# Optimization experiments

Measured on AMD Instinct MI355X. Metric: run time of the kernel, lower is better.

## Reference

```python
import jax, jax.numpy as jnp
import numpy as np

B, L, D_MODEL, N_HEADS = 8, 256, 2048, 8
D_HEAD = D_MODEL // N_HEADS  # 256 == L, required by DeltaRuleOperator broadcasting
ALPHA0, BETA0 = 0.1, 0.9      # delta_rule_strength, 1 - strength
LN_EPS = 1e-5


def setup_inputs() -> dict:
    k = jax.random.key(0)
    ks = jax.random.split(k, 8)
    s = 0.02
    return {
        "query": jax.random.normal(ks[0], (B, L, D_MODEL), jnp.float32),
        "key": jax.random.normal(ks[1], (B, L, D_MODEL), jnp.float32),
        "value": jax.random.normal(ks[2], (B, L, D_MODEL), jnp.float32),
        "Wq": jax.random.normal(ks[3], (D_MODEL, D_MODEL), jnp.float32) * s,
        "Wk": jax.random.normal(ks[4], (D_MODEL, D_MODEL), jnp.float32) * s,
        "Wv": jax.random.normal(ks[5], (D_MODEL, D_MODEL), jnp.float32) * s,
        "Wo": jax.random.normal(ks[6], (D_MODEL, D_MODEL), jnp.float32) * s,
        "bo": jnp.zeros((D_MODEL,), jnp.float32),
        "ln_g": jnp.ones((D_MODEL,), jnp.float32),
        "ln_b": jnp.zeros((D_MODEL,), jnp.float32),
        "alpha": jnp.asarray(ALPHA0, jnp.float32),
        "beta": jnp.asarray(BETA0, jnp.float32),
    }


def reference(query, key, value, Wq, Wk, Wv, Wo, bo, ln_g, ln_b, alpha, beta):
    Bs, Ls, D = query.shape
    H, Dh = N_HEADS, D // N_HEADS

    def proj(x, W):  # torch Linear: x @ W.T, split heads -> [B,H,L,Dh]
        return (x @ W.T).reshape(Bs, Ls, H, Dh).transpose(0, 2, 1, 3)

    Q = proj(query, Wq)
    K = proj(key, Wk)
    V = proj(value, Wv)

    # DeltaRuleOperator, applied sequentially per head (buffer mutates across heads)
    kv = jnp.einsum('bhld,bhmd->bhlm', K, V)  # [B,H,L,L] with L == Dh
    kv_heads = jnp.moveaxis(kv, 1, 0)          # [H,B,L,L]

    def cs_step(cs, kv_h):
        # cumulative_state = beta*cs + alpha*detach(mean(kv)); head uses pre-update cs
        new = beta * cs + alpha * jax.lax.stop_gradient(kv_h.mean(axis=(0, 1)))
        return new, cs

    _, cs_seq = jax.lax.scan(cs_step, jnp.zeros((Dh,), query.dtype), kv_heads)  # [H,Dh]
    cs_b = cs_seq[None, :, None, :]                       # [1,H,1,Dh]
    q_mod = Q * (cs_b + alpha * (kv - cs_b))              # delta-rule modulated queries

    # elu feature map
    phi = lambda x: jax.nn.elu(x) + 1.0
    pq, pk = phi(q_mod), phi(K)

    def time_major(x):  # [B,H,L,Dh] -> [L, B*H, Dh]
        return x.reshape(Bs * H, Ls, Dh).transpose(1, 0, 2)

    pq_t, pk_t, v_t = time_major(pq), time_major(pk), time_major(V)

    def step(carry, xs):
        S, Z = carry                        # S:[N,Dh,Dh], Z:[N,Dh]
        q_i, k_i, v_i = xs                  # each [N,Dh]
        S = S + k_i[:, :, None] * v_i[:, None, :]
        Z = Z + k_i
        num = jnp.einsum('nf,nfd->nd', q_i, S)
        den = jnp.maximum(jnp.sum(q_i * Z, axis=-1), 1e-8)
        return (S, Z), num / den[:, None]

    N = Bs * H
    S0 = jnp.zeros((N, Dh, Dh), query.dtype)
    Z0 = jnp.zeros((N, Dh), query.dtype)
    _, outs = jax.lax.scan(step, (S0, Z0), (pq_t, pk_t, v_t))  # [L,N,Dh]

    attn = outs.transpose(1, 0, 2).reshape(Bs, H, Ls, Dh)
    attn = attn.transpose(0, 2, 1, 3).reshape(Bs, Ls, D)       # concat heads

    o = attn @ Wo.T + bo                  # out_proj (dropout is identity in eval)
    x = query + o                          # residual + LayerNorm
    mu = x.mean(-1, keepdims=True)
    var = jnp.mean((x - mu) ** 2, axis=-1, keepdims=True)
    return (x - mu) / jnp.sqrt(var + LN_EPS) * ln_g + ln_b
```

## Files before the change

### kernel.cpp

```cpp
#include <hip/hip_runtime.h>
#include <hip/hip_bf16.h>

using u16 = unsigned short;

typedef __bf16 bf16x8 __attribute__((ext_vector_type(8)));
typedef float  f32x4  __attribute__((ext_vector_type(4)));

__device__ __forceinline__ float b2f(u16 u) {
  union { unsigned u; float f; } v; v.u = ((unsigned)u) << 16; return v.f;
}
__device__ __forceinline__ u16 f2b(float f) {
  union { float f; unsigned u; } v; v.f = f;
  unsigned r = v.u + 0x7fffu + ((v.u >> 16) & 1u);
  return (u16)(r >> 16);
}

__device__ __forceinline__ void gld_lds16(const void* g, void* l) {
  __builtin_amdgcn_global_load_lds(
      (__attribute__((address_space(1))) void*)(unsigned long long)(g),
      (__attribute__((address_space(3))) void*)(unsigned long long)(l),
      16, 0, 0);
}

template <int EPI>
__global__ __launch_bounds__(256) void gemm_bt(
    const u16* __restrict__ A, int lda, long sA1, long sA2,
    const u16* __restrict__ B, int ldb, long sB1, long sB2,
    void* __restrict__ Cv, int ldc, long sC1, long sC2,
    int K, int HDIV,
    const float* __restrict__ den, int denLd,
    const float* __restrict__ bias, const float* __restrict__ resid) {
  __shared__ __align__(16) u16 lds[8192];
  const int t = threadIdx.x;
  const int lane = t & 63;
  const int wave = t >> 6;
  const int wm = wave >> 1, wn = wave & 1;
  const int laneM = lane & 15, quad = lane >> 4;
  const int zb = blockIdx.z / HDIV, zh = blockIdx.z % HDIV;

  int bx = blockIdx.x, by = blockIdx.y;
  if (EPI == 2) { by = (bx >= 1) ? 1 : 0; bx = (bx == 2) ? 1 : 0; }
  const int kEnd = (EPI == 3) ? ((by + 1) * 128 < K ? (by + 1) * 128 : K) : K;

  const u16* Abase = A + zb * sA1 + zh * sA2 + (long)by * 128 * lda;
  const u16* Bbase = B + zb * sB1 + zh * sB2 + (long)bx * 128 * ldb;

  const int rA = t >> 2;
  const int kc = (((t & 3) ^ ((rA >> 1) & 3)) * 8);

  f32x4 acc[4][4];
#pragma unroll
  for (int i = 0; i < 4; ++i)
#pragma unroll
    for (int j = 0; j < 4; ++j) acc[i][j] = (f32x4){0.f, 0.f, 0.f, 0.f};

  const int fragOff = laneM * 32 + ((quad ^ ((laneM >> 1) & 3)) * 8);

  for (int k0 = 0; k0 < kEnd; k0 += 32) {
    gld_lds16(Abase + (long)rA * lda + k0 + kc, &lds[t * 8]);
    gld_lds16(Abase + (long)(rA + 64) * lda + k0 + kc, &lds[2048 + t * 8]);
    gld_lds16(Bbase + (long)rA * ldb + k0 + kc, &lds[4096 + t * 8]);
    gld_lds16(Bbase + (long)(rA + 64) * ldb + k0 + kc, &lds[6144 + t * 8]);
    __syncthreads();
    bf16x8 af[4], bfv[4];
#pragma unroll
    for (int i = 0; i < 4; ++i)
      af[i] = *(const bf16x8*)&lds[(wm * 64 + i * 16) * 32 + fragOff];
#pragma unroll
    for (int j = 0; j < 4; ++j)
      bfv[j] = *(const bf16x8*)&lds[4096 + (wn * 64 + j * 16) * 32 + fragOff];
#pragma unroll
    for (int i = 0; i < 4; ++i)
#pragma unroll
      for (int j = 0; j < 4; ++j)
        acc[i][j] = __builtin_amdgcn_mfma_f32_16x16x32_bf16(af[i], bfv[j],
                                                            acc[i][j], 0, 0, 0);
    __syncthreads();
  }

  const long cOff = zb * sC1 + zh * sC2;
  const int rowB = by * 128 + wm * 64;
  const int colB = bx * 128 + wn * 64;
#pragma unroll
  for (int i = 0; i < 4; ++i) {
#pragma unroll
    for (int j = 0; j < 4; ++j) {
#pragma unroll
      for (int r = 0; r < 4; ++r) {
        const int row = rowB + i * 16 + quad * 4 + r;
        const int col = colB + j * 16 + laneM;
        const long idx = cOff + (long)row * ldc + col;
        float v = acc[i][j][r];
        if (EPI == 0) {
          ((u16*)Cv)[idx] = f2b(v);
        } else if (EPI == 1) {
          ((float*)Cv)[idx] = v;
        } else if (EPI == 2) {
          ((u16*)Cv)[idx] = f2b(col <= row ? v : 0.0f);
        } else if (EPI == 3) {
          ((u16*)Cv)[idx] = f2b(v / den[(long)blockIdx.z * denLd + row]);
        } else {
          ((float*)Cv)[idx] = v + bias[col] + resid[(long)row * ldc + col];
        }
      }
    }
  }
}

__global__ __launch_bounds__(256) void convert7(
    const float* __restrict__ s0, const float* __restrict__ s1,
    const float* __restrict__ s2, const float* __restrict__ s3,
    const float* __restrict__ s4, const float* __restrict__ s5,
    const float* __restrict__ s6, u16* __restrict__ dst) {
  long idx = (long)blockIdx.x * 256 + threadIdx.x;
  int seg = (int)(idx >> 20);
  long off = (idx & 1048575) << 2;
  const float* s;
  switch (seg) {
    case 0: s = s0; break; case 1: s = s1; break; case 2: s = s2; break;
    case 3: s = s3; break; case 4: s = s4; break; case 5: s = s5; break;
    default: s = s6;
  }
  float4 v = *(const float4*)(s + off);
  ushort4 o;
  o.x = f2b(v.x); o.y = f2b(v.y); o.z = f2b(v.z); o.w = f2b(v.w);
  *(ushort4*)(dst + (long)seg * 4194304 + off) = o;
}

__global__ __launch_bounds__(256) void kv_mean_partial(
    const float* __restrict__ kv, float* __restrict__ part) {
  int h = blockIdx.x, chunk = blockIdx.y, m = threadIdx.x;
  float acc = 0.f;
  for (int g = chunk * 128; g < chunk * 128 + 128; ++g) {
    int b = g >> 8, l = g & 255;
    acc += kv[(((long)(b * 8 + h) * 256) + l) * 256 + m];
  }
  part[(h * 16 + chunk) * 256 + m] = acc;
}

__global__ __launch_bounds__(256) void cs_kernel(
    const float* __restrict__ part, float* __restrict__ cs,
    const float* __restrict__ alphaP, const float* __restrict__ betaP) {
  int m = threadIdx.x;
  float alpha = *alphaP, beta = *betaP;
  float c = 0.f;
  for (int h = 0; h < 8; ++h) {
    cs[h * 256 + m] = c;
    float s = 0.f;
    for (int ch = 0; ch < 16; ++ch) s += part[(h * 16 + ch) * 256 + m];
    c = beta * c + alpha * (s * (1.0f / 2048.0f));
  }
}

__global__ __launch_bounds__(256) void pqpk_kernel(
    const u16* __restrict__ Qp, const u16* __restrict__ Kp,
    const float* __restrict__ kv, const float* __restrict__ cs,
    const float* __restrict__ alphaP, u16* __restrict__ pq,
    u16* __restrict__ pk) {
  long idx = (long)blockIdx.x * 256 + threadIdx.x;
  int d = idx & 255, l = (int)((idx >> 8) & 255), h = (int)((idx >> 16) & 7),
      b = (int)(idx >> 19);
  float alpha = *alphaP;
  long pidx = ((long)(b * 256 + l)) * 2048 + h * 256 + d;
  float Qv = b2f(Qp[pidx]);
  float kvv = kv[idx];
  float csv = cs[h * 256 + d];
  float qm = Qv * (csv + alpha * (kvv - csv));
  pq[idx] = f2b(qm > 0.f ? qm + 1.f : expf(qm));
  float Kv = b2f(Kp[pidx]);
  pk[idx] = f2b(Kv > 0.f ? Kv + 1.f : expf(Kv));
}

__global__ __launch_bounds__(256) void den_kernel(const u16* __restrict__ Ab,
                                                  float* __restrict__ den) {
  int wave = threadIdx.x >> 6, lane = threadIdx.x & 63;
  int row = blockIdx.x * 4 + wave;
  int rloc = row & 255;
  ushort4 v = *(const ushort4*)(Ab + (long)row * 256 + lane * 4);
  int j = lane * 4;
  float s = (j <= rloc ? b2f(v.x) : 0.f) + (j + 1 <= rloc ? b2f(v.y) : 0.f) +
            (j + 2 <= rloc ? b2f(v.z) : 0.f) + (j + 3 <= rloc ? b2f(v.w) : 0.f);
  for (int o = 32; o; o >>= 1) s += __shfl_xor(s, o);
  if (lane == 0) den[row] = fmaxf(s, 1e-8f);
}

__global__ __launch_bounds__(256) void vtrans_kernel(const u16* __restrict__ Vp,
                                                     u16* __restrict__ Vt) {
  __shared__ u16 tile[32][33];
  int z = blockIdx.z, b = z >> 3, h = z & 7;
  int jT = blockIdx.x * 32, dT = blockIdx.y * 32;
  int tx = threadIdx.x, ty = threadIdx.y;
#pragma unroll
  for (int ii = 0; ii < 4; ++ii) {
    int j = jT + ty + ii * 8, d = dT + tx;
    tile[ty + ii * 8][tx] = Vp[(long)(b * 256 + j) * 2048 + h * 256 + d];
  }
  __syncthreads();
#pragma unroll
  for (int ii = 0; ii < 4; ++ii) {
    int d = dT + ty + ii * 8, j = jT + tx;
    Vt[(long)z * 65536 + d * 256 + j] = tile[tx][ty + ii * 8];
  }
}

__global__ __launch_bounds__(256) void ln_kernel(
    const float* __restrict__ x, const float* __restrict__ g,
    const float* __restrict__ bb, float* __restrict__ out) {
  int row = blockIdx.x, t = threadIdx.x;
  const float4* xr = (const float4*)(x + (long)row * 2048);
  float4 v0 = xr[t], v1 = xr[t + 256];
  float s = v0.x + v0.y + v0.z + v0.w + v1.x + v1.y + v1.z + v1.w;
  float ss = v0.x * v0.x + v0.y * v0.y + v0.z * v0.z + v0.w * v0.w +
             v1.x * v1.x + v1.y * v1.y + v1.z * v1.z + v1.w * v1.w;
  for (int o = 32; o; o >>= 1) { s += __shfl_xor(s, o); ss += __shfl_xor(ss, o); }
  __shared__ float a1[4], a2[4];
  int wave = t >> 6, lane = t & 63;
  if (lane == 0) { a1[wave] = s; a2[wave] = ss; }
  __syncthreads();
  s = a1[0] + a1[1] + a1[2] + a1[3];
  ss = a2[0] + a2[1] + a2[2] + a2[3];
  float mu = s * (1.f / 2048.f);
  float var = ss * (1.f / 2048.f) - mu * mu;
  float rstd = rsqrtf(var + 1e-5f);
  const float4* g4 = (const float4*)g;
  const float4* b4 = (const float4*)bb;
  float4* orow = (float4*)(out + (long)row * 2048);
  float4 gg = g4[t], bv = b4[t], r;
  r.x = (v0.x - mu) * rstd * gg.x + bv.x;
  r.y = (v0.y - mu) * rstd * gg.y + bv.y;
  r.z = (v0.z - mu) * rstd * gg.z + bv.z;
  r.w = (v0.w - mu) * rstd * gg.w + bv.w;
  orow[t] = r;
  gg = g4[t + 256]; bv = b4[t + 256];
  r.x = (v1.x - mu) * rstd * gg.x + bv.x;
  r.y = (v1.y - mu) * rstd * gg.y + bv.y;
  r.z = (v1.z - mu) * rstd * gg.z + bv.z;
  r.w = (v1.w - mu) * rstd * gg.w + bv.w;
  orow[t + 256] = r;
}

extern "C" void kernel_launch(void* const* d_in, const int* in_sizes, int n_in,
                              void* d_out, int out_size, void* d_ws,
                              size_t ws_size, hipStream_t stream) {
  const float* query = (const float*)d_in[0];
  const float* key = (const float*)d_in[1];
  const float* value = (const float*)d_in[2];
  const float* Wq = (const float*)d_in[3];
  const float* Wk = (const float*)d_in[4];
  const float* Wv = (const float*)d_in[5];
  const float* Wo = (const float*)d_in[6];
  const float* bo = (const float*)d_in[7];
  const float* ln_g = (const float*)d_in[8];
  const float* ln_b = (const float*)d_in[9];
  const float* alphaP = (const float*)d_in[10];
  const float* betaP = (const float*)d_in[11];

  char* ws = (char*)d_ws;
  const long SZ = 8388608;
  u16* qb = (u16*)(ws);
  u16* Wb = (u16*)(ws + 3 * SZ);
  u16* Qp = (u16*)(ws + 7 * SZ);
  float* kvf = (float*)(ws + 10 * SZ);
  u16* pq = (u16*)(ws + 12 * SZ);
  u16* pk = (u16*)(ws + 13 * SZ);
  u16* Vt = (u16*)(ws + 14 * SZ);
  u16* attnb = (u16*)(ws + 15 * SZ);
  u16* Ab = (u16*)(ws + 10 * SZ);
  float* x = (float*)(ws + 12 * SZ);
  float* den = (float*)(ws + 16 * SZ);
  float* part = (float*)(ws + 16 * SZ + 65536);
  float* cs = (float*)(ws + 16 * SZ + 65536 + 16384);

  u16* Kp = Qp + 4194304;
  u16* Vp = Qp + 8388608;
  u16* Wob = Wb + 3 * 4194304;

  convert7<<<28672, 256, 0, stream>>>(query, key, value, Wq, Wk, Wv, Wo, qb);

  gemm_bt<0><<<dim3(16, 16, 3), 256, 0, stream>>>(
      qb, 2048, 4194304L, 0L, Wb, 2048, 4194304L, 0L, (void*)Qp, 2048,
      4194304L, 0L, 2048, 1, nullptr, 0, nullptr, nullptr);

  gemm_bt<1><<<dim3(2, 2, 64), 256, 0, stream>>>(
      Kp, 2048, 524288L, 256L, Vp, 2048, 524288L, 256L, (void*)kvf, 256,
      524288L, 65536L, 256, 8, nullptr, 0, nullptr, nullptr);

  kv_mean_partial<<<dim3(8, 16), 256, 0, stream>>>(kvf, part);
  cs_kernel<<<1, 256, 0, stream>>>(part, cs, alphaP, betaP);

  pqpk_kernel<<<16384, 256, 0, stream>>>(Qp, Kp, kvf, cs, alphaP, pq, pk);

  gemm_bt<2><<<dim3(3, 1, 64), 256, 0, stream>>>(
      pq, 256, 524288L, 65536L, pk, 256, 524288L, 65536L, (void*)Ab, 256,
      524288L, 65536L, 256, 8, nullptr, 0, nullptr, nullptr);

  den_kernel<<<4096, 256, 0, stream>>>(Ab, den);

  vtrans_kernel<<<dim3(8, 8, 64), dim3(32, 8), 0, stream>>>(Vp, Vt);

  gemm_bt<3><<<dim3(2, 2, 64), 256, 0, stream>>>(
      Ab, 256, 524288L, 65536L, Vt, 256, 524288L, 65536L, (void*)attnb, 2048,
      524288L, 256L, 256, 8, den, 256, nullptr, nullptr);

  gemm_bt<4><<<dim3(16, 16, 1), 256, 0, stream>>>(
      attnb, 2048, 0L, 0L, Wob, 2048, 0L, 0L, (void*)x, 2048, 0L, 0L, 2048, 1,
      nullptr, 0, bo, query);

  ln_kernel<<<2048, 256, 0, stream>>>(x, ln_g, ln_b, (float*)d_out);
}
```

Baseline: 350.5 us.

## Use K=64 GEMM tiles, fuse the denominator into the attention GEMM, split-K the output projection

The GEMM's K-step grows from 32 to 64 with a wider LDS tile and an 8-way XOR swizzle, halving the number of barrier pairs per tile. The separate den_kernel is removed. The causal row sums of the attention matrix are now accumulated from A fragments inside the EPI=3 GEMM and reduced through shared memory. The out-projection becomes a 2-way split-K whose partials are summed in the LayerNorm kernel, giving more blocks at the cost of an extra fp32 buffer read and write.

After: 345.7 us. No clear change (-1.4%).

```diff
diff --git a/kernel.cpp b/kernel.cpp
--- a/kernel.cpp
+++ b/kernel.cpp
@@ -28,9 +28,9 @@
     const u16* __restrict__ B, int ldb, long sB1, long sB2,
     void* __restrict__ Cv, int ldc, long sC1, long sC2,
     int K, int HDIV,
-    const float* __restrict__ den, int denLd,
     const float* __restrict__ bias, const float* __restrict__ resid) {
-  __shared__ __align__(16) u16 lds[8192];
+  __shared__ __align__(16) u16 lds[16384];
+  __shared__ float denS[128];
   const int t = threadIdx.x;
   const int lane = t & 63;
   const int wave = t >> 6;
@@ -45,41 +45,76 @@
   const u16* Abase = A + zb * sA1 + zh * sA2 + (long)by * 128 * lda;
   const u16* Bbase = B + zb * sB1 + zh * sB2 + (long)bx * 128 * ldb;
 
-  const int rA = t >> 2;
-  const int kc = (((t & 3) ^ ((rA >> 1) & 3)) * 8);
+  const int sRow = t >> 3;
+  const int sc = ((t & 7) ^ (sRow & 7)) * 8;
 
   f32x4 acc[4][4];
 #pragma unroll
   for (int i = 0; i < 4; ++i)
 #pragma unroll
     for (int j = 0; j < 4; ++j) acc[i][j] = (f32x4){0.f, 0.f, 0.f, 0.f};
-
-  const int fragOff = laneM * 32 + ((quad ^ ((laneM >> 1) & 3)) * 8);
-
-  for (int k0 = 0; k0 < kEnd; k0 += 32) {
-    gld_lds16(Abase + (long)rA * lda + k0 + kc, &lds[t * 8]);
-    gld_lds16(Abase + (long)(rA + 64) * lda + k0 + kc, &lds[2048 + t * 8]);
-    gld_lds16(Bbase + (long)rA * ldb + k0 + kc, &lds[4096 + t * 8]);
-    gld_lds16(Bbase + (long)(rA + 64) * ldb + k0 + kc, &lds[6144 + t * 8]);
+  float dsum[4] = {0.f, 0.f, 0.f, 0.f};
+
+  const int fragA = (wm * 64 + laneM) * 64;
+  const int fragB = 8192 + (wn * 64 + laneM) * 64;
+  const int pbase = laneM & 7;
+
+  for (int k0 = 0; k0 < kEnd; k0 += 64) {
+#pragma unroll
+    for (int p = 0; p < 4; ++p)
+      gld_lds16(Abase + (long)(p * 32 + sRow) * lda + k0 + sc,
+                &lds[p * 2048 + t * 8]);
+#pragma unroll
+    for (int p = 0; p < 4; ++p)
+      gld_lds16(Bbase + (long)(p * 32 + sRow) * ldb + k0 + sc,
+                &lds[8192 + p * 2048 + t * 8]);
     __syncthreads();
-    bf16x8 af[4], bfv[4];
-#pragma unroll
-    for (int i = 0; i < 4; ++i)
-      af[i] = *(const bf16x8*)&lds[(wm * 64 + i * 16) * 32 + fragOff];
-#pragma unroll
-    for (int j = 0; j < 4; ++j)
-      bfv[j] = *(const bf16x8*)&lds[4096 + (wn * 64 + j * 16) * 32 + fragOff];
-#pragma unroll
-    for (int i = 0; i < 4; ++i)
-#pragma unroll
-      for (int j = 0; j < 4; ++j)
-        acc[i][j] = __builtin_amdgcn_mfma_f32_16x16x32_bf16(af[i], bfv[j],
-                                                            acc[i][j], 0, 0, 0);
+    bf16x8 af[2][4], bfv[2][4];
+#pragma unroll
+    for (int kk = 0; kk < 2; ++kk) {
+      const int perm8 = ((kk * 4 + quad) ^ pbase) * 8;
+#pragma unroll
+      for (int i = 0; i < 4; ++i) {
+        af[kk][i] = *(const bf16x8*)&lds[fragA + i * 1024 + perm8];
+        bfv[kk][i] = *(const bf16x8*)&lds[fragB + i * 1024 + perm8];
+      }
+    }
+    if (EPI == 3) {
+#pragma unroll
+      for (int kk = 0; kk < 2; ++kk)
+#pragma unroll
+        for (int i = 0; i < 4; ++i) {
+          union { bf16x8 v; u16 s[8]; } u; u.v = af[kk][i];
+          float ds = 0.f;
+#pragma unroll
+          for (int e = 0; e < 8; ++e) ds += b2f(u.s[e]);
+          dsum[i] += ds;
+        }
+    }
+#pragma unroll
+    for (int kk = 0; kk < 2; ++kk)
+#pragma unroll
+      for (int i = 0; i < 4; ++i)
+#pragma unroll
+        for (int j = 0; j < 4; ++j)
+          acc[i][j] = __builtin_amdgcn_mfma_f32_16x16x32_bf16(
+              af[kk][i], bfv[kk][j], acc[i][j], 0, 0, 0);
     __syncthreads();
   }
 
+  if (EPI == 3) {
+#pragma unroll
+    for (int i = 0; i < 4; ++i) {
+      float s = dsum[i];
+      s += __shfl_xor(s, 16);
+      s += __shfl_xor(s, 32);
+      if (wn == 0 && quad == 0)
+        denS[wm * 64 + i * 16 + laneM] = fmaxf(s, 1e-8f);
+    }
+    __syncthreads();
+  }
+
   const long cOff = zb * sC1 + zh * sC2;
-  const int rowB = by * 128 + wm * 64;
   const int colB = bx * 128 + wn * 64;
 #pragma unroll
   for (int i = 0; i < 4; ++i) {
@@ -87,7 +122,8 @@
     for (int j = 0; j < 4; ++j) {
 #pragma unroll
       for (int r = 0; r < 4; ++r) {
-        const int row = rowB + i * 16 + quad * 4 + r;
+        const int lrow = wm * 64 + i * 16 + quad * 4 + r;
+        const int row = by * 128 + lrow;
         const int col = colB + j * 16 + laneM;
         const long idx = cOff + (long)row * ldc + col;
         float v = acc[i][j][r];
@@ -98,9 +134,10 @@
         } else if (EPI == 2) {
           ((u16*)Cv)[idx] = f2b(col <= row ? v : 0.0f);
         } else if (EPI == 3) {
-          ((u16*)Cv)[idx] = f2b(v / den[(long)blockIdx.z * denLd + row]);
+          ((u16*)Cv)[idx] = f2b(v / denS[lrow]);
         } else {
-          ((float*)Cv)[idx] = v + bias[col] + resid[(long)row * ldc + col];
+          ((float*)Cv)[idx] =
+              (zb == 0) ? v + bias[col] + resid[(long)row * ldc + col] : v;
         }
       }
     }
@@ -171,19 +208,6 @@
   pk[idx] = f2b(Kv > 0.f ? Kv + 1.f : expf(Kv));
 }
 
-__global__ __launch_bounds__(256) void den_kernel(const u16* __restrict__ Ab,
-                                                  float* __restrict__ den) {
-  int wave = threadIdx.x >> 6, lane = threadIdx.x & 63;
-  int row = blockIdx.x * 4 + wave;
-  int rloc = row & 255;
-  ushort4 v = *(const ushort4*)(Ab + (long)row * 256 + lane * 4);
-  int j = lane * 4;
-  float s = (j <= rloc ? b2f(v.x) : 0.f) + (j + 1 <= rloc ? b2f(v.y) : 0.f) +
-            (j + 2 <= rloc ? b2f(v.z) : 0.f) + (j + 3 <= rloc ? b2f(v.w) : 0.f);
-  for (int o = 32; o; o >>= 1) s += __shfl_xor(s, o);
-  if (lane == 0) den[row] = fmaxf(s, 1e-8f);
-}
-
 __global__ __launch_bounds__(256) void vtrans_kernel(const u16* __restrict__ Vp,
                                                      u16* __restrict__ Vt) {
   __shared__ u16 tile[32][33];
@@ -204,21 +228,26 @@
 }
 
 __global__ __launch_bounds__(256) void ln_kernel(
-    const float* __restrict__ x, const float* __restrict__ g,
-    const float* __restrict__ bb, float* __restrict__ out) {
+    const float* __restrict__ x0, const float* __restrict__ x1,
+    const float* __restrict__ g, const float* __restrict__ bb,
+    float* __restrict__ out) {
   int row = blockIdx.x, t = threadIdx.x;
-  const float4* xr = (const float4*)(x + (long)row * 2048);
-  float4 v0 = xr[t], v1 = xr[t + 256];
+  const float4* xr0 = (const float4*)(x0 + (long)row * 2048);
+  const float4* xr1 = (const float4*)(x1 + (long)row * 2048);
+  float4 a0 = xr0[t], b0 = xr1[t], a1 = xr0[t + 256], b1 = xr1[t + 256];
+  float4 v0, v1;
+  v0.x = a0.x + b0.x; v0.y = a0.y + b0.y; v0.z = a0.z + b0.z; v0.w = a0.w + b0.w;
+  v1.x = a1.x + b1.x; v1.y = a1.y + b1.y; v1.z = a1.z + b1.z; v1.w = a1.w + b1.w;
   float s = v0.x + v0.y + v0.z + v0.w + v1.x + v1.y + v1.z + v1.w;
   float ss = v0.x * v0.x + v0.y * v0.y + v0.z * v0.z + v0.w * v0.w +
              v1.x * v1.x + v1.y * v1.y + v1.z * v1.z + v1.w * v1.w;
   for (int o = 32; o; o >>= 1) { s += __shfl_xor(s, o); ss += __shfl_xor(ss, o); }
-  __shared__ float a1[4], a2[4];
+  __shared__ float a1s[4], a2s[4];
   int wave = t >> 6, lane = t & 63;
-  if (lane == 0) { a1[wave] = s; a2[wave] = ss; }
+  if (lane == 0) { a1s[wave] = s; a2s[wave] = ss; }
   __syncthreads();
-  s = a1[0] + a1[1] + a1[2] + a1[3];
-  ss = a2[0] + a2[1] + a2[2] + a2[3];
+  s = a1s[0] + a1s[1] + a1s[2] + a1s[3];
+  ss = a2s[0] + a2s[1] + a2s[2] + a2s[3];
   float mu = s * (1.f / 2048.f);
   float var = ss * (1.f / 2048.f) - mu * mu;
   float rstd = rsqrtf(var + 1e-5f);
@@ -266,10 +295,10 @@
   u16* Vt = (u16*)(ws + 14 * SZ);
   u16* attnb = (u16*)(ws + 15 * SZ);
   u16* Ab = (u16*)(ws + 10 * SZ);
-  float* x = (float*)(ws + 12 * SZ);
-  float* den = (float*)(ws + 16 * SZ);
-  float* part = (float*)(ws + 16 * SZ + 65536);
-  float* cs = (float*)(ws + 16 * SZ + 65536 + 16384);
+  float* x0 = (float*)(ws + 12 * SZ);
+  float* x1 = (float*)(ws);
+  float* part = (float*)(ws + 16 * SZ);
+  float* cs = (float*)(ws + 16 * SZ + 16384);
 
   u16* Kp = Qp + 4194304;
   u16* Vp = Qp + 8388608;
@@ -279,11 +308,11 @@
 
   gemm_bt<0><<<dim3(16, 16, 3), 256, 0, stream>>>(
       qb, 2048, 4194304L, 0L, Wb, 2048, 4194304L, 0L, (void*)Qp, 2048,
-      4194304L, 0L, 2048, 1, nullptr, 0, nullptr, nullptr);
+      4194304L, 0L, 2048, 1, nullptr, nullptr);
 
   gemm_bt<1><<<dim3(2, 2, 64), 256, 0, stream>>>(
       Kp, 2048, 524288L, 256L, Vp, 2048, 524288L, 256L, (void*)kvf, 256,
-      524288L, 65536L, 256, 8, nullptr, 0, nullptr, nullptr);
+      524288L, 65536L, 256, 8, nullptr, nullptr);
 
   kv_mean_partial<<<dim3(8, 16), 256, 0, stream>>>(kvf, part);
   cs_kernel<<<1, 256, 0, stream>>>(part, cs, alphaP, betaP);
@@ -292,19 +321,17 @@
 
   gemm_bt<2><<<dim3(3, 1, 64), 256, 0, stream>>>(
       pq, 256, 524288L, 65536L, pk, 256, 524288L, 65536L, (void*)Ab, 256,
-      524288L, 65536L, 256, 8, nullptr, 0, nullptr, nullptr);
-
-  den_kernel<<<4096, 256, 0, stream>>>(Ab, den);
+      524288L, 65536L, 256, 8, nullptr, nullptr);
 
   vtrans_kernel<<<dim3(8, 8, 64), dim3(32, 8), 0, stream>>>(Vp, Vt);
 
   gemm_bt<3><<<dim3(2, 2, 64), 256, 0, stream>>>(
       Ab, 256, 524288L, 65536L, Vt, 256, 524288L, 65536L, (void*)attnb, 2048,
-      524288L, 256L, 256, 8, den, 256, nullptr, nullptr);
-
-  gemm_bt<4><<<dim3(16, 16, 1), 256, 0, stream>>>(
-      attnb, 2048, 0L, 0L, Wob, 2048, 0L, 0L, (void*)x, 2048, 0L, 0L, 2048, 1,
-      nullptr, 0, bo, query);
-
-  ln_kernel<<<2048, 256, 0, stream>>>(x, ln_g, ln_b, (float*)d_out);
-}
+      524288L, 256L, 256, 8, nullptr, nullptr);
+
+  gemm_bt<4><<<dim3(16, 16, 2), 256, 0, stream>>>(
+      attnb, 2048, 1024L, 0L, Wob, 2048, 1024L, 0L, (void*)x0, 2048,
+      -25165824L, 0L, 1024, 1, bo, query);
+
+  ln_kernel<<<2048, 256, 0, stream>>>(x0, x1, ln_g, ln_b, (float*)d_out);
+}
```
